# Kernel tuning notes

Hardware: AMD Instinct MI355X
Metric: run time of the kernel (lower is better)

## Reference

```python
import jax, jax.numpy as jnp
import numpy as np

N, C, H, W = 32, 256, 56, 56   # batch, channels (inplanes == planes), spatial
EPS = 1e-5                     # BatchNorm eps (PyTorch default)
THR = 0.5                      # mask_hard_threshold (hard_inference mode)


def conv3x3(x, w):
    # stride 1, padding 1, no bias -- matches conv3x3() in the source
    return jax.lax.conv_general_dilated(
        x, w, window_strides=(1, 1), padding=((1, 1), (1, 1)),
        dimension_numbers=('NCHW', 'OIHW', 'NCHW'))


def bn_inf(y, g, b, mu, v):
    # inference-mode BatchNorm: per-channel affine with running stats
    s = (g * jax.lax.rsqrt(v + EPS))[None, :, None, None]
    return y * s + (b - mu * g * jax.lax.rsqrt(v + EPS))[None, :, None, None]


def setup_inputs() -> dict:
    key = jax.random.key(0)
    ks = jax.random.split(key, 10)
    x = jax.random.normal(ks[0], (N, C, H, W), jnp.float32)
    # main conv weights (3x3, no bias)
    w1 = jax.random.normal(ks[1], (C, C, 3, 3), jnp.float32) * 0.05
    w2 = jax.random.normal(ks[2], (C, C, 3, 3), jnp.float32) * 0.05
    # BN params (running stats)
    g1 = jnp.ones((C,), jnp.float32); b1 = jnp.zeros((C,), jnp.float32)
    mu1 = jax.random.normal(ks[3], (C,), jnp.float32) * 0.1
    v1 = jax.random.uniform(ks[4], (C,), jnp.float32, 0.5, 1.5)
    g2 = jnp.ones((C,), jnp.float32); b2 = jnp.zeros((C,), jnp.float32)
    mu2 = jax.random.normal(ks[5], (C,), jnp.float32) * 0.1
    v2 = jax.random.uniform(ks[6], (C,), jnp.float32, 0.5, 1.5)
    # mask convs: Conv2d(C, 1, 3, stride=1, pad=1) with bias; random weights so the
    wm1 = jax.random.normal(ks[7], (1, C, 3, 3), jnp.float32) * 0.05
    bm1 = jnp.zeros((1,), jnp.float32)
    wm2 = jax.random.normal(ks[8], (1, C, 3, 3), jnp.float32) * 0.05
    bm2 = jnp.zeros((1,), jnp.float32)
    return dict(x=x, w1=w1, w2=w2, g1=g1, b1=b1, mu1=mu1, v1=v1,
                g2=g2, b2=b2, mu2=mu2, v2=v2,
                wm1=wm1, bm1=bm1, wm2=wm2, bm2=bm2)


def reference(x, w1, w2, g1, b1, mu1, v1, g2, b2, mu2, v2, wm1, bm1, wm2, bm2):
    # Gumbel-Sigmoid gates in hard_inference mode: sigmoid(mask_conv(x)) > threshold.
    # [N,1,H,W] hard masks (non-differentiable constants w.r.t. the gate).
    m1 = (jax.nn.sigmoid(conv3x3(x, wm1) + bm1[None, :, None, None]) > THR).astype(x.dtype)
    m2 = (jax.nn.sigmoid(conv3x3(x, wm2) + bm2[None, :, None, None]) > THR).astype(x.dtype)
    # apply_proxy_dcn_bn_relu: gather patches at mask_loc -> matmul(W) -> BN -> ReLU
    # -> scatter (zeros elsewhere). Dense-equivalent: relu(bn(conv(x))) * mask.
    out = jax.nn.relu(bn_inf(conv3x3(x, w1), g1, b1, mu1, v1)) * m1
    # second conv: gather -> matmul -> BN -> scatter (ReLU applied after residual)
    out = bn_inf(conv3x3(out, w2), g2, b2, mu2, v2) * m2
    # residual add (identity: stride=1, inplanes==planes -> no downsample) + ReLU
    return jax.nn.relu(out + x)
```

## Files before the change

### kernel.cpp

```cpp
#include <hip/hip_runtime.h>
#include <hip/hip_bf16.h>


#define NB 32
#define C  256
#define H  56
#define W  56
#define HW (H*W)
#define NBHW (NB*HW)
#define EPSV 1e-5f
#define WELEM (C*C*9)
#define MSPL 2
#define MCH (C/MSPL)

typedef __hip_bfloat16 bf16;
typedef __attribute__((ext_vector_type(8))) short  bf16x8;
typedef __attribute__((ext_vector_type(4))) float  floatx4;

__global__ __launch_bounds__(128) void wcvt_kernel(
    const float* __restrict__ wm1, const float* __restrict__ wm2,
    double* __restrict__ wd)
{
    int i = blockIdx.x * 128 + threadIdx.x;
    if (i >= C * 18) return;
    int c = i / 18;
    int r = i - c * 18;
    int m = r / 9;
    int t = r - 9 * m;
    const float* src = m ? wm2 : wm1;
    wd[i] = (double)src[c * 9 + t];
}

__global__ __launch_bounds__(128) void mask_part_kernel(
    const float* __restrict__ x, const double* __restrict__ wd,
    double* __restrict__ z)
{
    int pixb  = blockIdx.x >> 1;
    int split = blockIdx.x & 1;
    int idx = pixb * 128 + threadIdx.x;
    int n  = idx / HW;
    int hw = idx - n * HW;

    const float*  xp = x  + (size_t)n * C * HW + (size_t)split * MCH * HW + hw;
    const double* wp = wd + (size_t)split * MCH * 18;

    double acc[18];
    #pragma unroll
    for (int j = 0; j < 18; ++j) acc[j] = 0.0;

    for (int c = 0; c < MCH; ++c) {
        double xv = (double)xp[(size_t)c * HW];
        const double* w = wp + c * 18;
        #pragma unroll
        for (int j = 0; j < 18; ++j)
            acc[j] += xv * w[j];
    }

    #pragma unroll
    for (int j = 0; j < 18; ++j)
        z[(size_t)(split * 18 + j) * NBHW + idx] = acc[j];
}

__global__ __launch_bounds__(256) void mask_reduce_kernel(
    const double* __restrict__ z,
    const float* __restrict__ bm1, const float* __restrict__ bm2,
    float* __restrict__ m1, float* __restrict__ m2)
{
    int idx = blockIdx.x * 256 + threadIdx.x;
    int n  = idx / HW;
    int hw = idx - n * HW;
    int h  = hw / W;
    int w_ = hw - h * W;

    double a1 = (double)bm1[0], a2 = (double)bm2[0];
    #pragma unroll
    for (int ky = 0; ky < 3; ++ky) {
        int y = h + ky - 1;
        if ((unsigned)y >= (unsigned)H) continue;
        #pragma unroll
        for (int kx = 0; kx < 3; ++kx) {
            int xx = w_ + kx - 1;
            if ((unsigned)xx >= (unsigned)W) continue;
            int t = ky * 3 + kx;
            size_t q = (size_t)n * HW + (size_t)y * W + xx;
            a1 += z[(size_t)(0 * 18 + 0 * 9 + t) * NBHW + q]
                + z[(size_t)(1 * 18 + 0 * 9 + t) * NBHW + q];
            a2 += z[(size_t)(0 * 18 + 1 * 9 + t) * NBHW + q]
                + z[(size_t)(1 * 18 + 1 * 9 + t) * NBHW + q];
        }
    }
    m1[idx] = (a1 > 0.0) ? 1.0f : 0.0f;
    m2[idx] = (a2 > 0.0) ? 1.0f : 0.0f;
}

__global__ __launch_bounds__(256) void transpose_kernel(
    const float* __restrict__ x, bf16* __restrict__ xb)
{
    __shared__ float tile[64][65];
    int bid = blockIdx.x;
    int pt = bid % 49; bid /= 49;
    int ct = bid % 4;  int n = bid / 4;
    int p0 = pt * 64, c0 = ct * 64;
    int tl = threadIdx.x & 63;
    int tg = threadIdx.x >> 6;
    const float* xp = x + ((size_t)(n*C + c0) * HW) + p0;
    #pragma unroll
    for (int i = 0; i < 16; ++i) {
        int cl = tg*16 + i;
        tile[cl][tl] = xp[(size_t)cl * HW + tl];
    }
    __syncthreads();
    bf16* op = xb + ((size_t)(n*HW + p0) * C) + c0;
    #pragma unroll
    for (int i = 0; i < 16; ++i) {
        int pl = tg*16 + i;
        op[(size_t)pl * C + tl] = __float2bfloat16(tile[tl][pl]);
    }
}

__global__ __launch_bounds__(256) void pack_kernel(
    const float* __restrict__ w1, const float* __restrict__ w2,
    bf16* __restrict__ w1p, bf16* __restrict__ w2p)
{
    int idx = blockIdx.x * 256 + threadIdx.x;
    const float* src = (idx < WELEM) ? w1 : w2;
    bf16* dst        = (idx < WELEM) ? w1p : w2p;
    int f = (idx < WELEM) ? idx : idx - WELEM;
    int e  = f & 7;
    int O  = f >> 3;
    int L  = O & 63;
    int j  = (O >> 6) & 15;
    int ks = (O >> 10) & 7;
    int t  = O >> 13;
    int co = j*16 + (L & 15);
    int ci = ks*32 + ((L >> 4) & 3)*8 + e;
    dst[f] = __float2bfloat16(src[((size_t)co*C + ci)*9 + t]);
}

template<bool FIRST>
__global__ __launch_bounds__(256, 3) void conv_mfma(
    const bf16* __restrict__ inb,
    const bf16* __restrict__ wp,
    const float* __restrict__ g,  const float* __restrict__ b,
    const float* __restrict__ mu, const float* __restrict__ vv,
    const float* __restrict__ mask,
    const float* __restrict__ xres,
    bf16* __restrict__ outb,
    float* __restrict__ outf)
{
    __shared__ uint4 patch4[1700];
    __shared__ float msk[64];
    short* patch = (short*)patch4;

    int bid  = blockIdx.x;
    int tile = bid % 49;
    int n    = bid / 49;
    int y0 = (tile / 7) * 8;
    int x0 = (tile % 7) * 8;

    int tid = threadIdx.x;
    int L   = tid & 63;
    int wv  = tid >> 6;

    if (tid < 64) {
        int pr = tid >> 3, pc = tid & 7;
        msk[tid] = mask[(size_t)n*HW + (y0+pr)*W + (x0+pc)];
    }

    int m  = L & 15;
    int kb = L >> 4;
    int abase[4];
    #pragma unroll
    for (int mi = 0; mi < 4; ++mi) {
        int p   = mi*16 + m;
        int pos = (p >> 3)*10 + (p & 7);
        abase[mi] = pos*136 + kb*8;
    }

    floatx4 acc[4][4];
    #pragma unroll
    for (int mi = 0; mi < 4; ++mi)
        #pragma unroll
        for (int jj = 0; jj < 4; ++jj)
            acc[mi][jj] = (floatx4){0.f, 0.f, 0.f, 0.f};

    const size_t img_base = (size_t)n * HW * C;

    for (int ck = 0; ck < 2; ++ck) {
        if (ck) __syncthreads();
        for (int S = tid; S < 1600; S += 256) {
            int q   = S & 15;
            int pos = S >> 4;
            int r = pos / 10, c = pos - (pos/10)*10;
            int y  = y0 + r - 1;
            int xx = x0 + c - 1;
            uint4 val = make_uint4(0u, 0u, 0u, 0u);
            if ((unsigned)y < (unsigned)H && (unsigned)xx < (unsigned)W)
                val = *(const uint4*)(inb + img_base + (size_t)(y*W + xx)*C + ck*128 + q*8);
            patch4[pos*17 + q] = val;
        }
        __syncthreads();

        bf16x8 bcur[4], bnxt[4];
        bf16x8 acur[4], anxt[4];
        {
            int ks0 = ck*4;
            #pragma unroll
            for (int jj = 0; jj < 4; ++jj) {
                int jgl = wv*4 + jj;
                bcur[jj] = *(const bf16x8*)(wp + ((size_t)((0*8 + ks0)*16 + jgl)*64 + L)*8);
            }
            #pragma unroll
            for (int mi = 0; mi < 4; ++mi)
                acur[mi] = *(const bf16x8*)(patch + abase[mi]);
        }
        for (int gs = 0; gs < 36; ++gs) {
            if (gs < 35) {
                int g2 = gs + 1;
                int t2 = g2 >> 2, s2 = g2 & 3;
                int ks2 = ck*4 + s2;
                #pragma unroll
                for (int jj = 0; jj < 4; ++jj) {
                    int jgl = wv*4 + jj;
                    bnxt[jj] = *(const bf16x8*)(wp + ((size_t)((t2*8 + ks2)*16 + jgl)*64 + L)*8);
                }
                int ky2 = t2 / 3;
                int dt2 = ky2*10 + (t2 - ky2*3);
                int aoff2 = dt2*136 + s2*32;
                #pragma unroll
                for (int mi = 0; mi < 4; ++mi)
                    anxt[mi] = *(const bf16x8*)(patch + abase[mi] + aoff2);
            }
            #pragma unroll
            for (int mi = 0; mi < 4; ++mi)
                #pragma unroll
                for (int jj = 0; jj < 4; ++jj)
                    acc[mi][jj] = __builtin_amdgcn_mfma_f32_16x16x32_bf16(
                        acur[mi], bcur[jj], acc[mi][jj], 0, 0, 0);
            #pragma unroll
            for (int jj = 0; jj < 4; ++jj) bcur[jj] = bnxt[jj];
            #pragma unroll
            for (int mi = 0; mi < 4; ++mi) acur[mi] = anxt[mi];
        }
    }

    int quad  = L >> 4;
    int wbase = wv * 64;
    #pragma unroll
    for (int jj = 0; jj < 4; ++jj) {
        int co = wbase + jj*16 + (L & 15);
        float s_ = g[co] * rsqrtf(vv[co] + EPSV);
        float t_ = b[co] - mu[co] * s_;
        #pragma unroll
        for (int mi = 0; mi < 4; ++mi) {
            int pbase = mi*16 + quad*4;
            if (FIRST) {
                #pragma unroll
                for (int r = 0; r < 4; ++r) {
                    int p = pbase + r;
                    float v = acc[mi][jj][r] * s_ + t_;
                    v = fmaxf(v, 0.f) * msk[p];
                    int pg = (y0 + (p >> 3))*W + (x0 + (p & 7));
                    outb[img_base + (size_t)pg*C + co] = __float2bfloat16(v);
                }
            } else {
                int pg = (y0 + (pbase >> 3))*W + (x0 + (pbase & 7));
                size_t oidx = ((size_t)(n*C + co))*HW + pg;
                floatx4 xr = *(const floatx4*)(xres + oidx);
                floatx4 ov;
                #pragma unroll
                for (int r = 0; r < 4; ++r) {
                    float v = acc[mi][jj][r] * s_ + t_;
                    v = v * msk[pbase + r] + xr[r];
                    ov[r] = fmaxf(v, 0.f);
                }
                *(floatx4*)(outf + oidx) = ov;
            }
        }
    }
}

extern "C" void kernel_launch(void* const* d_in, const int* in_sizes, int n_in,
                              void* d_out, int out_size, void* d_ws, size_t ws_size,
                              hipStream_t stream) {
    const float* x   = (const float*)d_in[0];
    const float* w1  = (const float*)d_in[1];
    const float* w2  = (const float*)d_in[2];
    const float* g1  = (const float*)d_in[3];
    const float* b1  = (const float*)d_in[4];
    const float* mu1 = (const float*)d_in[5];
    const float* v1  = (const float*)d_in[6];
    const float* g2  = (const float*)d_in[7];
    const float* b2  = (const float*)d_in[8];
    const float* mu2 = (const float*)d_in[9];
    const float* v2  = (const float*)d_in[10];
    const float* wm1 = (const float*)d_in[11];
    const float* bm1 = (const float*)d_in[12];
    const float* wm2 = (const float*)d_in[13];
    const float* bm2 = (const float*)d_in[14];
    float* out = (float*)d_out;

    float* m1   = (float*)d_ws;
    float* m2   = m1 + (size_t)NBHW;
    bf16*  w1p  = (bf16*)(m2 + (size_t)NBHW);
    bf16*  w2p  = w1p + WELEM;
    bf16*  tmpb = w2p + WELEM;
    double* z   = (double*)(tmpb + (size_t)NBHW*C);
    double* wd  = z + (size_t)MSPL*18*NBHW;
    bf16*  xb   = (bf16*)d_out;

    wcvt_kernel<<<(C*18 + 127)/128, 128, 0, stream>>>(wm1, wm2, wd);
    mask_part_kernel<<<(NBHW/128)*MSPL, 128, 0, stream>>>(x, wd, z);
    mask_reduce_kernel<<<NBHW/256, 256, 0, stream>>>(z, bm1, bm2, m1, m2);
    transpose_kernel<<<NB*4*49, 256, 0, stream>>>(x, xb);
    pack_kernel<<<2*WELEM/256, 256, 0, stream>>>(w1, w2, w1p, w2p);

    const int grid = NB * 49;
    conv_mfma<true ><<<grid, 256, 0, stream>>>(
        xb,   w1p, g1, b1, mu1, v1, m1, nullptr, tmpb, nullptr);
    conv_mfma<false><<<grid, 256, 0, stream>>>(
        tmpb, w2p, g2, b2, mu2, v2, m2, x, nullptr, out);
}
```

Before: 557.6 us.

## Process two 8x8 spatial tiles per block to reuse weight fragments

```diff
diff --git a/kernel.cpp b/kernel.cpp
--- a/kernel.cpp
+++ b/kernel.cpp
@@ -138,7 +138,7 @@
 }
 
 template<bool FIRST>
-__global__ __launch_bounds__(256, 3) void conv_mfma(
+__global__ __launch_bounds__(256, 2) void conv_mfma(
     const bf16* __restrict__ inb,
     const bf16* __restrict__ wp,
     const float* __restrict__ g,  const float* __restrict__ b,
@@ -148,61 +148,73 @@
     bf16* __restrict__ outb,
     float* __restrict__ outf)
 {
-    __shared__ uint4 patch4[1700];
-    __shared__ float msk[64];
+    __shared__ uint4 patch4[3400];
+    __shared__ float msk[128];
     short* patch = (short*)patch4;
-
-    int bid  = blockIdx.x;
-    int tile = bid % 49;
-    int n    = bid / 49;
-    int y0 = (tile / 7) * 8;
-    int x0 = (tile % 7) * 8;
 
     int tid = threadIdx.x;
     int L   = tid & 63;
     int wv  = tid >> 6;
 
-    if (tid < 64) {
-        int pr = tid >> 3, pc = tid & 7;
-        msk[tid] = mask[(size_t)n*HW + (y0+pr)*W + (x0+pc)];
+    int t0g = blockIdx.x * 2;
+    int n_s[2], y0_s[2], x0_s[2];
+    size_t ibase_s[2];
+    #pragma unroll
+    for (int s = 0; s < 2; ++s) {
+        int ts = t0g + s;
+        int ns = ts / 49;
+        int tl = ts - ns * 49;
+        n_s[s]  = ns;
+        y0_s[s] = (tl / 7) * 8;
+        x0_s[s] = (tl % 7) * 8;
+        ibase_s[s] = (size_t)ns * HW * C;
+    }
+
+    if (tid < 128) {
+        int s  = tid >> 6;
+        int p  = tid & 63;
+        int pr = p >> 3, pc = p & 7;
+        msk[tid] = mask[(size_t)n_s[s]*HW + (y0_s[s]+pr)*W + (x0_s[s]+pc)];
     }
 
     int m  = L & 15;
     int kb = L >> 4;
-    int abase[4];
-    #pragma unroll
-    for (int mi = 0; mi < 4; ++mi) {
+    int abase[8];
+    #pragma unroll
+    for (int mi = 0; mi < 8; ++mi) {
         int p   = mi*16 + m;
-        int pos = (p >> 3)*10 + (p & 7);
-        abase[mi] = pos*136 + kb*8;
-    }
-
-    floatx4 acc[4][4];
-    #pragma unroll
-    for (int mi = 0; mi < 4; ++mi)
+        int s   = p >> 6;
+        int pl  = p & 63;
+        int pos = (pl >> 3)*10 + (pl & 7);
+        abase[mi] = s*13600 + pos*136 + kb*8;
+    }
+
+    floatx4 acc[8][4];
+    #pragma unroll
+    for (int mi = 0; mi < 8; ++mi)
         #pragma unroll
         for (int jj = 0; jj < 4; ++jj)
             acc[mi][jj] = (floatx4){0.f, 0.f, 0.f, 0.f};
 
-    const size_t img_base = (size_t)n * HW * C;
-
     for (int ck = 0; ck < 2; ++ck) {
         if (ck) __syncthreads();
-        for (int S = tid; S < 1600; S += 256) {
-            int q   = S & 15;
-            int pos = S >> 4;
-            int r = pos / 10, c = pos - (pos/10)*10;
-            int y  = y0 + r - 1;
-            int xx = x0 + c - 1;
+        for (int S = tid; S < 3200; S += 256) {
+            int s   = S >= 1600;
+            int r0  = S - s*1600;
+            int q   = r0 & 15;
+            int pos = r0 >> 4;
+            int rr = pos / 10, cc = pos - (pos/10)*10;
+            int y  = y0_s[s] + rr - 1;
+            int xx = x0_s[s] + cc - 1;
             uint4 val = make_uint4(0u, 0u, 0u, 0u);
             if ((unsigned)y < (unsigned)H && (unsigned)xx < (unsigned)W)
-                val = *(const uint4*)(inb + img_base + (size_t)(y*W + xx)*C + ck*128 + q*8);
-            patch4[pos*17 + q] = val;
+                val = *(const uint4*)(inb + ibase_s[s] + (size_t)(y*W + xx)*C + ck*128 + q*8);
+            patch4[s*1700 + pos*17 + q] = val;
         }
         __syncthreads();
 
         bf16x8 bcur[4], bnxt[4];
-        bf16x8 acur[4], anxt[4];
+        bf16x8 acur[8], anxt[8];
         {
             int ks0 = ck*4;
             #pragma unroll
@@ -211,7 +223,7 @@
                 bcur[jj] = *(const bf16x8*)(wp + ((size_t)((0*8 + ks0)*16 + jgl)*64 + L)*8);
             }
             #pragma unroll
-            for (int mi = 0; mi < 4; ++mi)
+            for (int mi = 0; mi < 8; ++mi)
                 acur[mi] = *(const bf16x8*)(patch + abase[mi]);
         }
         for (int gs = 0; gs < 36; ++gs) {
@@ -228,11 +240,11 @@
                 int dt2 = ky2*10 + (t2 - ky2*3);
                 int aoff2 = dt2*136 + s2*32;
                 #pragma unroll
-                for (int mi = 0; mi < 4; ++mi)
+                for (int mi = 0; mi < 8; ++mi)
                     anxt[mi] = *(const bf16x8*)(patch + abase[mi] + aoff2);
             }
             #pragma unroll
-            for (int mi = 0; mi < 4; ++mi)
+            for (int mi = 0; mi < 8; ++mi)
                 #pragma unroll
                 for (int jj = 0; jj < 4; ++jj)
                     acc[mi][jj] = __builtin_amdgcn_mfma_f32_16x16x32_bf16(
@@ -240,7 +252,7 @@
             #pragma unroll
             for (int jj = 0; jj < 4; ++jj) bcur[jj] = bnxt[jj];
             #pragma unroll
-            for (int mi = 0; mi < 4; ++mi) acur[mi] = anxt[mi];
+            for (int mi = 0; mi < 8; ++mi) acur[mi] = anxt[mi];
         }
     }
 
@@ -252,20 +264,22 @@
         float s_ = g[co] * rsqrtf(vv[co] + EPSV);
         float t_ = b[co] - mu[co] * s_;
         #pragma unroll
-        for (int mi = 0; mi < 4; ++mi) {
+        for (int mi = 0; mi < 8; ++mi) {
             int pbase = mi*16 + quad*4;
+            int s   = pbase >> 6;
+            int pl  = pbase & 63;
             if (FIRST) {
                 #pragma unroll
                 for (int r = 0; r < 4; ++r) {
-                    int p = pbase + r;
+                    int p = pl + r;
                     float v = acc[mi][jj][r] * s_ + t_;
-                    v = fmaxf(v, 0.f) * msk[p];
-                    int pg = (y0 + (p >> 3))*W + (x0 + (p & 7));
-                    outb[img_base + (size_t)pg*C + co] = __float2bfloat16(v);
+                    v = fmaxf(v, 0.f) * msk[pbase + r];
+                    int pg = (y0_s[s] + (p >> 3))*W + (x0_s[s] + (p & 7));
+                    outb[ibase_s[s] + (size_t)pg*C + co] = __float2bfloat16(v);
                 }
             } else {
-                int pg = (y0 + (pbase >> 3))*W + (x0 + (pbase & 7));
-                size_t oidx = ((size_t)(n*C + co))*HW + pg;
+                int pg = (y0_s[s] + (pl >> 3))*W + (x0_s[s] + (pl & 7));
+                size_t oidx = ((size_t)(n_s[s]*C + co))*HW + pg;
                 floatx4 xr = *(const floatx4*)(xres + oidx);
                 floatx4 ov;
                 #pragma unroll
@@ -315,7 +329,7 @@
     transpose_kernel<<<NB*4*49, 256, 0, stream>>>(x, xb);
     pack_kernel<<<2*WELEM/256, 256, 0, stream>>>(w1, w2, w1p, w2p);
 
-    const int grid = NB * 49;
+    const int grid = NBHW / 128;
     conv_mfma<true ><<<grid, 256, 0, stream>>>(
         xb,   w1p, g1, b1, mu1, v1, m1, nullptr, tmpb, nullptr);
     conv_mfma<false><<<grid, 256, 0, stream>>>(
```

Result: no change. 549.6 us (-1.4%).
